# Performance work log

Measured on AMD Instinct MI355X. Metric: run time of the kernel, lower is better.

## Reference

```python
import jax, jax.numpy as jnp
import numpy as np

# Model dims
B = 64            # scenes (memory batch)
APER = 16         # agents per scene (uniform `length`)
A = B * APER      # total agents = sum(length)
TPAST = 20
TFUT = 30         # len_future
C = 256           # controller_size
M = 128           # memory_m
N = 256           # memory_n
H = 5             # num_heads (future modes)
SPACE = N // APER # per-agent write slot band
EMB = 16
D = C + M         # decoder hidden size


def _gru(x, h, wih, whh, bih, bhh):
    """torch.nn.GRU single-cell step."""
    gi = x @ wih.T + bih
    gh = h @ whh.T + bhh
    ir, iz, inn = jnp.split(gi, 3, axis=-1)
    hr, hz, hn = jnp.split(gh, 3, axis=-1)
    r = jax.nn.sigmoid(ir + hr)
    z = jax.nn.sigmoid(iz + hz)
    n = jnp.tanh(inn + r * hn)
    return (1.0 - z) * n + z * h


def _address(k, beta, mem, mask):
    """NTM content addressing: beta-sharpened masked softmax over cosine sims.
    k: (...,B,APER,M), beta: (...,B,APER,1), mem: (B,N,M), mask: (APER,N)."""
    kn = k / (jnp.linalg.norm(k, axis=-1, keepdims=True) + 1e-16)
    mn = mem / (jnp.linalg.norm(mem, axis=-1, keepdims=True) + 1e-16)
    sim = jnp.einsum('...bam,bnm->...ban', kn, mn)
    logits = beta * sim + (mask - 1.0) * 1e9
    return jax.nn.softmax(logits, axis=-1)


def setup_inputs() -> dict:
    key = jax.random.key(0)
    ks = iter(jax.random.split(key, 64))
    def nrm(shape, scale):
        return jax.random.normal(next(ks), shape, dtype=jnp.float32) * scale
    inp = dict(
        past=nrm((A, TPAST, 2), 1.0),
        past_rel=nrm((A, TPAST, 2), 1.0),
        ep_w1=nrm((8, 2), 0.7), ep_b1=jnp.zeros(8), ep_w2=nrm((EMB, 8), 0.35), ep_b2=jnp.zeros(EMB),
        er_w1=nrm((8, 2), 0.7), er_b1=jnp.zeros(8), er_w2=nrm((EMB, 8), 0.35), er_b2=jnp.zeros(EMB),
        enc_wih=nrm((3 * C, EMB + M), 1.0 / np.sqrt(EMB + M)), enc_whh=nrm((3 * C, C), 1.0 / np.sqrt(C)),
        enc_bih=jnp.zeros(3 * C), enc_bhh=jnp.zeros(3 * C),
        rel_wih=nrm((3 * C, EMB), 1.0 / np.sqrt(EMB)), rel_whh=nrm((3 * C, C), 1.0 / np.sqrt(C)),
        rel_bih=jnp.zeros(3 * C), rel_bhh=jnp.zeros(3 * C),
        dec_wih=nrm((3 * D, D), 1.0 / np.sqrt(D)), dec_whh=nrm((3 * D, D), 1.0 / np.sqrt(D)),
        dec_bih=jnp.zeros(3 * D), dec_bhh=jnp.zeros(3 * D),
        out_w=nrm((2, D), 1.0 / np.sqrt(D)), out_b=jnp.zeros(2),
        read_w=nrm((H, M + 1, C), 1.0 / np.sqrt(C)), read_b=jnp.zeros((H, M + 1)),
        write_w=nrm((3 * M + 1, C), 1.0 / np.sqrt(C)), write_b=jnp.zeros(3 * M + 1),
        init_r=nrm((1, M), 0.01),
        h_bias=nrm((1, C), 0.05), h_rel_bias=nrm((1, C), 0.05), h_fut_bias=nrm((1, D), 0.05),
        mem_bias=nrm((N, M), 0.05),
    )
    return inp


def reference(past, past_rel, ep_w1, ep_b1, ep_w2, ep_b2, er_w1, er_b1, er_w2, er_b2,
              enc_wih, enc_whh, enc_bih, enc_bhh, rel_wih, rel_whh, rel_bih, rel_bhh,
              dec_wih, dec_whh, dec_bih, dec_bhh, out_w, out_b,
              read_w, read_b, write_w, write_b,
              init_r, h_bias, h_rel_bias, h_fut_bias, mem_bias):
    # Per-agent disjoint write bands; read mask = other agents' bands.
    owner = jnp.arange(N) // SPACE
    mask_w = (owner[None, :] == jnp.arange(APER)[:, None]).astype(jnp.float32)  # (APER,N)
    mask_r = 1.0 - mask_w

    def mlp(x, w1, b1, w2, b2):
        return jax.nn.relu(x @ w1.T + b1) @ w2.T + b2

    emb_p = jnp.transpose(mlp(past, ep_w1, ep_b1, ep_w2, ep_b2), (1, 0, 2))      # (T,A,16)
    emb_r = jnp.transpose(mlp(past_rel, er_w1, er_b1, er_w2, er_b2), (1, 0, 2))  # (T,A,16)

    def step(carry, xs):
        emb, embr = xs
        mem, h, hr, hf, r = carry
        h = _gru(jnp.concatenate([emb, r], axis=-1), h, enc_wih, enc_whh, enc_bih, enc_bhh)
        hr = _gru(embr, hr, rel_wih, rel_whh, rel_bih, rel_bhh)
        # write head: k, beta, erase, add
        wp = h @ write_w.T + write_b
        kw = jnp.tanh(wp[:, :M]).reshape(B, APER, M)
        betaw = jax.nn.softplus(wp[:, M:M + 1]).reshape(B, APER, 1)
        er = jax.nn.sigmoid(wp[:, M + 1:2 * M + 1]).reshape(B, APER, M)
        ad = jnp.tanh(wp[:, 2 * M + 1:]).reshape(B, APER, M)
        ww = _address(kw, betaw, mem, mask_w)                                    # (B,APER,N)
        # erase/add; write bands are disjoint across agents so aggregation is exact
        mem = mem * (1.0 - jnp.einsum('ban,bam->bnm', ww, er)) + jnp.einsum('ban,bam->bnm', ww, ad)
        # per-head reads
        rp = jnp.einsum('ac,hkc->hak', hr, read_w) + read_b[:, None, :]          # (H,A,M+1)
        kr = jnp.tanh(rp[..., :M]).reshape(H, B, APER, M)
        betar = jax.nn.softplus(rp[..., M:]).reshape(H, B, APER, 1)
        wr = _address(kr, betar, mem, mask_r)                                    # (H,B,APER,N)
        reads = jnp.einsum('hban,bnm->hbam', wr, mem).reshape(H, A, M)
        r = reads[0]
        # per-mode decoder
        dec_in = jnp.concatenate([jnp.broadcast_to(h[None], (H, A, C)), reads], axis=-1).reshape(H * A, D)
        hf = _gru(dec_in, hf, dec_wih, dec_whh, dec_bih, dec_bhh)
        out = (hf @ out_w.T + out_b).reshape(H, A, 2)
        return (mem, h, hr, hf, r), out

    carry0 = (jnp.broadcast_to(mem_bias[None], (B, N, M)),
              jnp.broadcast_to(h_bias, (A, C)),
              jnp.broadcast_to(h_rel_bias, (A, C)),
              jnp.broadcast_to(h_fut_bias, (H * A, D)),
              jnp.broadcast_to(init_r, (A, M)))
    carry, _ = jax.lax.scan(step, carry0, (emb_p, emb_r))
    zf = jnp.zeros((TFUT, A, EMB), dtype=past.dtype)
    carry, outs = jax.lax.scan(step, carry, (zf, zf))                            # (TFUT,H,A,2)
    pred_rel = jnp.transpose(outs, (2, 1, 0, 3))                                 # (A,H,TFUT,2)
    pred = past[:, -1][:, None, None, :] + jnp.cumsum(pred_rel, axis=2)
    return pred, pred_rel
```

## Files before the change

### kernel.cpp

```cpp
#include <hip/hip_runtime.h>
#include <math.h>

#define B_    64
#define APER_ 16
#define A_    1024
#define TPAST_ 20
#define TFUT_  30
#define C_    256
#define M_    128
#define N_    256
#define H_    5
#define EMB_  16
#define D_    384
#define TTOT_ 50

typedef short bf16x8 __attribute__((ext_vector_type(8)));
typedef float f32x4 __attribute__((ext_vector_type(4)));

__device__ __forceinline__ float sigmoidf_(float x) { return 1.0f / (1.0f + expf(-x)); }
__device__ __forceinline__ float softplusf_(float x) { return (x > 20.0f) ? x : log1pf(expf(x)); }
__device__ __forceinline__ unsigned short f2bf(float f) {
    unsigned u = __float_as_uint(f);
    return (unsigned short)((u + 0x7FFFu + ((u >> 16) & 1u)) >> 16);
}
__device__ __forceinline__ float bf2f(short s) {
    return __uint_as_float(((unsigned)(unsigned short)s) << 16);
}

struct Cvt { const float* src; short* dst; int rows, sk, dk, total; };
struct Cvt8 { Cvt c[8]; };

__global__ __launch_bounds__(256) void convert_all(Cvt8 p)
{
    const int stride = gridDim.x * 256;
    #pragma unroll
    for (int s = 0; s < 8; ++s) {
        const Cvt d = p.c[s];
        for (int idx = blockIdx.x * 256 + threadIdx.x; idx < d.total; idx += stride) {
            const int r = idx / d.dk, k = idx % d.dk;
            float v = (k < d.sk && r < d.rows) ? d.src[(size_t)r * d.sk + k] : 0.f;
            d.dst[idx] = (short)f2bf(v);
        }
    }
}

__global__ __launch_bounds__(256) void embed2_k(const float* __restrict__ past, const float* __restrict__ past_rel,
                                                const float* __restrict__ pw1, const float* __restrict__ pb1,
                                                const float* __restrict__ pw2, const float* __restrict__ pb2,
                                                const float* __restrict__ rw1, const float* __restrict__ rb1,
                                                const float* __restrict__ rw2, const float* __restrict__ rb2,
                                                short* __restrict__ emb_p, short* __restrict__ emb_r)
{
    const int idx0 = blockIdx.x * 256 + threadIdx.x;
    const int half = A_ * TPAST_;
    if (idx0 >= 2 * half) return;
    const bool second = idx0 >= half;
    const int idx = second ? idx0 - half : idx0;
    const float* x = second ? past_rel : past;
    const float* w1 = second ? rw1 : pw1; const float* b1 = second ? rb1 : pb1;
    const float* w2 = second ? rw2 : pw2; const float* b2 = second ? rb2 : pb2;
    short* emb = second ? emb_r : emb_p;

    const int a = idx / TPAST_, t = idx % TPAST_;
    const float x0 = x[(size_t)idx * 2], x1 = x[(size_t)idx * 2 + 1];
    float hbuf[8];
    #pragma unroll
    for (int j = 0; j < 8; ++j) hbuf[j] = fmaxf(0.f, w1[j * 2] * x0 + w1[j * 2 + 1] * x1 + b1[j]);
    short* e = emb + ((size_t)t * A_ + a) * EMB_;
    #pragma unroll
    for (int i = 0; i < 16; ++i) {
        float acc = b2[i];
        #pragma unroll
        for (int j = 0; j < 8; ++j) acc += w2[i * 8 + j] * hbuf[j];
        e[i] = (short)f2bf(acc);
    }
}

__global__ __launch_bounds__(256) void init_k(float* __restrict__ h, const float* __restrict__ h_bias, short* __restrict__ hb,
                                              float* __restrict__ hr, const float* __restrict__ hr_bias, short* __restrict__ hrb,
                                              const float* __restrict__ hf_bias, short* __restrict__ hfb,
                                              short* __restrict__ reads_b, const float* __restrict__ init_r,
                                              short* __restrict__ memhi, short* __restrict__ memlo,
                                              float* __restrict__ normsG, const float* __restrict__ mem_bias)
{
    const int idx = blockIdx.x * 256 + threadIdx.x;
    if (idx < B_ * N_ * M_) {
        const float v = mem_bias[idx & (N_ * M_ - 1)];
        const short hv = (short)f2bf(v);
        memhi[idx] = hv;
        memlo[idx] = (short)f2bf(v - bf2f(hv));
    }
    if (idx < B_ * N_) {
        const float* r = mem_bias + (size_t)(idx & (N_ - 1)) * M_;
        float ss = 0.f;
        for (int k = 0; k < M_; ++k) ss += r[k] * r[k];
        normsG[idx] = sqrtf(ss) + 1e-16f;
    }
    if (idx < A_ * C_) {
        float v = h_bias[idx & (C_ - 1)];
        h[idx] = v; hb[idx] = (short)f2bf(v);
        v = hr_bias[idx & (C_ - 1)];
        hr[idx] = v; hrb[idx] = (short)f2bf(v);
    }
    if (idx < H_ * A_ * D_) {
        hfb[idx] = (short)f2bf(hf_bias[idx % D_]);
    }
    if (idx < A_ * M_) reads_b[idx] = (short)f2bf(init_r[idx & (M_ - 1)]);
}

__device__ __forceinline__ void gru_tile_split(
    int role, float* __restrict__ xchLane,
    const short* __restrict__ X1, int K1,
    const short* __restrict__ X2, int K2,
    const short* __restrict__ Wih, int Kpad,
    const float* __restrict__ bih,
    const short* __restrict__ Hb, const short* __restrict__ Whh,
    const float* __restrict__ bhh,
    const float* __restrict__ Hprev,
    float* __restrict__ Hnew, short* __restrict__ Hnewb,
    int G, int rowBase, int colBase, int lane)
{
    const int l16 = lane & 15;
    const int kb8 = (lane >> 4) * 8;
    const f32x4 z4 = {0.f, 0.f, 0.f, 0.f};
    f32x4 a0[2][2], a1[2][2], a2[2][2];
    #pragma unroll
    for (int i = 0; i < 2; ++i)
        #pragma unroll
        for (int j = 0; j < 2; ++j) { a0[i][j] = z4; a1[i][j] = z4; a2[i][j] = z4; }

    if (role == 0) {
        for (int kc = 0; kc < Kpad; kc += 32) {
            const int k8 = kc + kb8;
            bf16x8 ax[2];
            #pragma unroll
            for (int i = 0; i < 2; ++i) {
                const int r = rowBase + i * 16 + l16;
                bf16x8 v = {0, 0, 0, 0, 0, 0, 0, 0};
                if (k8 < K1) {
                    if (X1) v = *(const bf16x8*)(X1 + (size_t)(r & 1023) * K1 + k8);
                } else if (k8 < K1 + K2) {
                    v = *(const bf16x8*)(X2 + (size_t)r * K2 + (k8 - K1));
                }
                ax[i] = v;
            }
            #pragma unroll
            for (int j = 0; j < 2; ++j) {
                const size_t wb = (size_t)(colBase + j * 16 + l16) * Kpad + k8;
                const bf16x8 b0 = *(const bf16x8*)(Wih + wb);
                const bf16x8 b1 = *(const bf16x8*)(Wih + (size_t)G * Kpad + wb);
                const bf16x8 b2 = *(const bf16x8*)(Wih + (size_t)2 * G * Kpad + wb);
                a0[0][j] = __builtin_amdgcn_mfma_f32_16x16x32_bf16(ax[0], b0, a0[0][j], 0, 0, 0);
                a0[1][j] = __builtin_amdgcn_mfma_f32_16x16x32_bf16(ax[1], b0, a0[1][j], 0, 0, 0);
                a1[0][j] = __builtin_amdgcn_mfma_f32_16x16x32_bf16(ax[0], b1, a1[0][j], 0, 0, 0);
                a1[1][j] = __builtin_amdgcn_mfma_f32_16x16x32_bf16(ax[1], b1, a1[1][j], 0, 0, 0);
                a2[0][j] = __builtin_amdgcn_mfma_f32_16x16x32_bf16(ax[0], b2, a2[0][j], 0, 0, 0);
                a2[1][j] = __builtin_amdgcn_mfma_f32_16x16x32_bf16(ax[1], b2, a2[1][j], 0, 0, 0);
            }
        }
        #pragma unroll
        for (int i = 0; i < 2; ++i)
            #pragma unroll
            for (int j = 0; j < 2; ++j)
                #pragma unroll
                for (int q = 0; q < 4; ++q) {
                    const int base = (i * 2 + j) * 4 + q;
                    xchLane[base]      = a0[i][j][q];
                    xchLane[16 + base] = a1[i][j][q];
                    xchLane[32 + base] = a2[i][j][q];
                }
    } else {
        for (int kc = 0; kc < G; kc += 32) {
            const int k8 = kc + kb8;
            bf16x8 ah[2];
            #pragma unroll
            for (int i = 0; i < 2; ++i)
                ah[i] = *(const bf16x8*)(Hb + (size_t)(rowBase + i * 16 + l16) * G + k8);
            #pragma unroll
            for (int j = 0; j < 2; ++j) {
                const size_t wb = (size_t)(colBase + j * 16 + l16) * G + k8;
                const bf16x8 b0 = *(const bf16x8*)(Whh + wb);
                const bf16x8 b1 = *(const bf16x8*)(Whh + (size_t)G * G + wb);
                const bf16x8 b2 = *(const bf16x8*)(Whh + (size_t)2 * G * G + wb);
                a0[0][j] = __builtin_amdgcn_mfma_f32_16x16x32_bf16(ah[0], b0, a0[0][j], 0, 0, 0);
                a0[1][j] = __builtin_amdgcn_mfma_f32_16x16x32_bf16(ah[1], b0, a0[1][j], 0, 0, 0);
                a1[0][j] = __builtin_amdgcn_mfma_f32_16x16x32_bf16(ah[0], b1, a1[0][j], 0, 0, 0);
                a1[1][j] = __builtin_amdgcn_mfma_f32_16x16x32_bf16(ah[1], b1, a1[1][j], 0, 0, 0);
                a2[0][j] = __builtin_amdgcn_mfma_f32_16x16x32_bf16(ah[0], b2, a2[0][j], 0, 0, 0);
                a2[1][j] = __builtin_amdgcn_mfma_f32_16x16x32_bf16(ah[1], b2, a2[1][j], 0, 0, 0);
            }
        }
    }
    __syncthreads();
    if (role != 1) return;

    const int r4 = (lane >> 4) * 4;
    #pragma unroll
    for (int j = 0; j < 2; ++j) {
        const int col = colBase + j * 16 + l16;
        const float b0c = bih[col] + bhh[col];
        const float b1c = bih[G + col] + bhh[G + col];
        const float bi2 = bih[2 * G + col], bh2 = bhh[2 * G + col];
        #pragma unroll
        for (int i = 0; i < 2; ++i) {
            #pragma unroll
            for (int q = 0; q < 4; ++q) {
                const int row = rowBase + i * 16 + r4 + q;
                const int base = (i * 2 + j) * 4 + q;
                const float arv = a0[i][j][q] + xchLane[base];
                const float azv = a1[i][j][q] + xchLane[16 + base];
                const float aniv = xchLane[32 + base];
                const float anhv = a2[i][j][q];
                const float rr = sigmoidf_(arv + b0c);
                const float zz = sigmoidf_(azv + b1c);
                const float nn = tanhf(aniv + bi2 + rr * (anhv + bh2));
                const float hp = Hprev ? Hprev[(size_t)row * G + col]
                                       : bf2f(Hb[(size_t)row * G + col]);
                const float hv = (1.f - zz) * nn + zz * hp;
                if (Hnew) Hnew[(size_t)row * G + col] = hv;
                Hnewb[(size_t)row * G + col] = (short)f2bf(hv);
            }
        }
    }
}

__device__ __forceinline__ void gemm_tile(
    const short* __restrict__ Xb, const short* __restrict__ Wb,
    const float* __restrict__ bias, float* __restrict__ Out,
    int Ncols, int K, int rowBase, int colBase, int lane)
{
    const int l16 = lane & 15;
    const int kb8 = (lane >> 4) * 8;
    const f32x4 z4 = {0.f, 0.f, 0.f, 0.f};
    f32x4 acc[2][2] = {{z4, z4}, {z4, z4}};

    for (int kc = 0; kc < K; kc += 32) {
        const int k8 = kc + kb8;
        const bf16x8 a0 = *(const bf16x8*)(Xb + (size_t)(rowBase + l16) * K + k8);
        const bf16x8 a1 = *(const bf16x8*)(Xb + (size_t)(rowBase + 16 + l16) * K + k8);
        const bf16x8 b0 = *(const bf16x8*)(Wb + (size_t)(colBase + l16) * K + k8);
        const bf16x8 b1 = *(const bf16x8*)(Wb + (size_t)(colBase + 16 + l16) * K + k8);
        acc[0][0] = __builtin_amdgcn_mfma_f32_16x16x32_bf16(a0, b0, acc[0][0], 0, 0, 0);
        acc[0][1] = __builtin_amdgcn_mfma_f32_16x16x32_bf16(a0, b1, acc[0][1], 0, 0, 0);
        acc[1][0] = __builtin_amdgcn_mfma_f32_16x16x32_bf16(a1, b0, acc[1][0], 0, 0, 0);
        acc[1][1] = __builtin_amdgcn_mfma_f32_16x16x32_bf16(a1, b1, acc[1][1], 0, 0, 0);
    }
    const int r4 = (lane >> 4) * 4;
    #pragma unroll
    for (int j = 0; j < 2; ++j) {
        const int col = colBase + j * 16 + l16;
        if (col >= Ncols) continue;
        const float bv = bias[col];
        #pragma unroll
        for (int i = 0; i < 2; ++i)
            #pragma unroll
            for (int q = 0; q < 4; ++q) {
                const int row = rowBase + i * 16 + r4 + q;
                Out[(size_t)row * Ncols + col] = acc[i][j][q] + bv;
            }
    }
}

__global__ __launch_bounds__(256) void phaseA(
    const short* __restrict__ ep, const short* __restrict__ er,
    const short* __restrict__ enc_wih, const float* __restrict__ enc_bih,
    const short* __restrict__ enc_whh, const float* __restrict__ enc_bhh,
    const short* __restrict__ rel_wih, const float* __restrict__ rel_bih,
    const short* __restrict__ rel_whh, const float* __restrict__ rel_bhh,
    const short* __restrict__ dec_wih, const float* __restrict__ dec_bih,
    const short* __restrict__ dec_whh, const float* __restrict__ dec_bhh,
    const float* __restrict__ hc, const short* __restrict__ hbc,
    float* __restrict__ hn, short* __restrict__ hbn,
    const float* __restrict__ hrc, const short* __restrict__ hrbc,
    float* __restrict__ hrn, short* __restrict__ hrbn,
    const short* __restrict__ hfbc, short* __restrict__ hfbn,
    const short* __restrict__ reads_b,
    int decBlocks, int encBlocks)
{
    __shared__ float xch[2][64][49];
    const int bid = blockIdx.x;
    const int wv = threadIdx.x >> 6;
    const int lane = threadIdx.x & 63;
    const int pair = wv >> 1, role = wv & 1;
    float* xchLane = &xch[pair][lane][0];

    if (bid < decBlocks) {
        const int tile = bid * 2 + pair;
        gru_tile_split(role, xchLane,
                       hbc, 256, reads_b, 128, dec_wih, 384, dec_bih,
                       hfbc, dec_whh, dec_bhh, nullptr, nullptr, hfbn, D_,
                       (tile / 12) * 32, (tile % 12) * 32, lane);
    } else if (bid < decBlocks + encBlocks) {
        const int tile = (bid - decBlocks) * 2 + pair;
        gru_tile_split(role, xchLane,
                       ep, 16, reads_b, 128, enc_wih, 160, enc_bih,
                       hbc, enc_whh, enc_bhh, hc, hn, hbn, C_,
                       (tile >> 3) * 32, (tile & 7) * 32, lane);
    } else {
        const int tile = (bid - decBlocks - encBlocks) * 2 + pair;
        gru_tile_split(role, xchLane,
                       er, 16, nullptr, 0, rel_wih, 32, rel_bih,
                       hrbc, rel_whh, rel_bhh, hrc, hrn, hrbn, C_,
                       (tile >> 3) * 32, (tile & 7) * 32, lane);
    }
}

__global__ __launch_bounds__(256) void phaseHeads(
    const short* __restrict__ hbn, const short* __restrict__ write_w_b,
    const float* __restrict__ write_b, float* __restrict__ wp,
    const short* __restrict__ hrbn, const short* __restrict__ read_w_b,
    const float* __restrict__ read_b, float* __restrict__ rp,
    const short* __restrict__ hfbn, const float* __restrict__ out_w,
    const float* __restrict__ out_b, float* __restrict__ predrel,
    int outT, int wpBlocks, int rpBlocks)
{
    const int bid = blockIdx.x;
    const int wave = threadIdx.x >> 6;
    const int lane = threadIdx.x & 63;

    if (bid < wpBlocks) {
        const int tile = bid * 4 + wave;
        gemm_tile(hbn, write_w_b, write_b, wp, 385, C_,
                  (tile & 31) * 32, (tile >> 5) * 32, lane);
    } else if (bid < wpBlocks + rpBlocks) {
        const int tile = (bid - wpBlocks) * 4 + wave;
        gemm_tile(hrbn, read_w_b, read_b, rp, 645, C_,
                  (tile & 31) * 32, (tile >> 5) * 32, lane);
    } else {
        const int widx = (bid - wpBlocks - rpBlocks) * 4 + wave;
        const int g = lane >> 3, li = lane & 7;
        const int row = widx * 8 + g;
        const short* hrow = hfbn + (size_t)row * D_;
        float a0 = 0.f, a1 = 0.f;
        #pragma unroll
        for (int u = 0; u < 6; ++u) {
            const int k0 = u * 64 + li * 8;
            const bf16x8 v = *(const bf16x8*)(hrow + k0);
            #pragma unroll
            for (int r = 0; r < 8; ++r) {
                const float f = bf2f(v[r]);
                a0 = fmaf(f, out_w[k0 + r], a0);
                a1 = fmaf(f, out_w[D_ + k0 + r], a1);
            }
        }
        a0 += __shfl_xor(a0, 1); a0 += __shfl_xor(a0, 2); a0 += __shfl_xor(a0, 4);
        a1 += __shfl_xor(a1, 1); a1 += __shfl_xor(a1, 2); a1 += __shfl_xor(a1, 4);
        if (li == 0) {
            const int hh = row >> 10, aa = row & 1023;
            float* o = predrel + (((size_t)aa * H_ + hh) * TFUT_ + outT) * 2;
            o[0] = a0 + out_b[0];
            o[1] = a1 + out_b[1];
        }
    }
}

__global__ __launch_bounds__(256) void write_mem_k(const float* __restrict__ wp,
                                                   short* __restrict__ memhi, short* __restrict__ memlo,
                                                   float* __restrict__ normsG)
{
    const int a = blockIdx.x;
    const int b = a >> 4, p = a & 15;
    __shared__ float kw[128], er[128], ad[128], red[256], ww[16], logit[16];
    __shared__ float buf[2048];
    __shared__ float beta_s, knorm_s;
    const int tid = threadIdx.x;
    const float* w = wp + (size_t)a * 385;
    if (tid < 128) {
        kw[tid] = tanhf(w[tid]);
        er[tid] = sigmoidf_(w[129 + tid]);
        ad[tid] = tanhf(w[257 + tid]);
    }
    if (tid == 0) beta_s = softplusf_(w[128]);
    __syncthreads();

    red[tid] = (tid < 128) ? kw[tid] * kw[tid] : 0.f;
    __syncthreads();
    for (int s = 128; s > 0; s >>= 1) { if (tid < s) red[tid] += red[tid + s]; __syncthreads(); }
    if (tid == 0) knorm_s = sqrtf(red[0]) + 1e-16f;
    __syncthreads();

    const int s = tid >> 4, j = tid & 15;
    float dot = 0.f, ss = 0.f;
    {
        const size_t row = (size_t)(b * N_) + p * 16 + s;
        const short* hi = memhi + row * M_;
        const short* lo = memlo + row * M_;
        for (int k = j; k < 128; k += 16) {
            const float v = bf2f(hi[k]) + bf2f(lo[k]);
            dot += kw[k] * v; ss += v * v;
        }
    }
    red[tid] = dot; __syncthreads();
    for (int st = 8; st > 0; st >>= 1) { if (j < st) red[tid] += red[tid + st]; __syncthreads(); }
    float dotf = red[s * 16];
    __syncthreads();
    red[tid] = ss; __syncthreads();
    for (int st = 8; st > 0; st >>= 1) { if (j < st) red[tid] += red[tid + st]; __syncthreads(); }
    float ssf = red[s * 16];
    if (j == 0) {
        float mn = sqrtf(ssf) + 1e-16f;
        logit[s] = beta_s * (dotf / (mn * knorm_s));
    }
    __syncthreads();
    if (tid == 0) {
        float mx = -1e30f;
        for (int i = 0; i < 16; ++i) mx = fmaxf(mx, logit[i]);
        float sum = 0.f;
        for (int i = 0; i < 16; ++i) { float e = __expf(logit[i] - mx); ww[i] = e; sum += e; }
        float inv = 1.f / sum;
        for (int i = 0; i < 16; ++i) ww[i] *= inv;
    }
    __syncthreads();
    for (int idx = tid; idx < 16 * 128; idx += 256) {
        int si = idx >> 7, m = idx & 127;
        size_t g = ((size_t)(b * N_) + p * 16 + si) * M_ + m;
        float wwv = ww[si];
        const float old = bf2f(memhi[g]) + bf2f(memlo[g]);
        float v = old * (1.f - wwv * er[m]) + wwv * ad[m];
        const short hv = (short)f2bf(v);
        memhi[g] = hv;
        memlo[g] = (short)f2bf(v - bf2f(hv));
        buf[idx] = v;
    }
    __syncthreads();
    {
        float ssq = 0.f;
        #pragma unroll
        for (int i = 0; i < 8; ++i) { float v = buf[s * 128 + j + 16 * i]; ssq += v * v; }
        #pragma unroll
        for (int m = 1; m < 16; m <<= 1) ssq += __shfl_xor(ssq, m);
        if (j == 0) normsG[b * N_ + p * 16 + s] = sqrtf(ssq) + 1e-16f;
    }
}

__global__ __launch_bounds__(256) void read_k2(const float* __restrict__ rp,
                                               const short* __restrict__ memhi,
                                               const short* __restrict__ memlo,
                                               const float* __restrict__ normsG,
                                               short* __restrict__ reads_b)
{
    const int b = blockIdx.x;
    const int h = blockIdx.y;
    __shared__ __align__(16) float kq[16 * 132];
    __shared__ float S[16 * 260];
    __shared__ float beta_s[16], knorm_s[16], inv_s[16];
    const int t = threadIdx.x;
    const int a = t >> 4;
    const int sub = t & 15;

    {
        const float* base = rp + ((size_t)(b * 16 + a)) * 645 + h * 129;
        const int k0 = sub * 8;
        float v[8]; float ss = 0.f;
        #pragma unroll
        for (int r = 0; r < 8; ++r) { v[r] = tanhf(base[k0 + r]); ss += v[r] * v[r]; }
        float* dst = kq + a * 132 + k0;
        *(float4*)dst = make_float4(v[0], v[1], v[2], v[3]);
        *(float4*)(dst + 4) = make_float4(v[4], v[5], v[6], v[7]);
        #pragma unroll
        for (int m = 1; m < 16; m <<= 1) ss += __shfl_xor(ss, m);
        if (sub == 0) {
            knorm_s[a] = sqrtf(ss) + 1e-16f;
            beta_s[a] = softplusf_(base[128]);
        }
    }
    __syncthreads();

    {
        const int wave = t >> 6, lane = t & 63;
        const int l16 = lane & 15, kb8 = (lane >> 4) * 8;
        const int slotBase = wave * 64;
        const f32x4 z4 = {0.f, 0.f, 0.f, 0.f};
        f32x4 acc[4] = {z4, z4, z4, z4};
        const short* mbh = memhi + (size_t)b * N_ * M_;
        const short* mbl = memlo + (size_t)b * N_ * M_;
        #pragma unroll
        for (int kc = 0; kc < 128; kc += 32) {
            const float* ap = kq + l16 * 132 + kc + kb8;
            bf16x8 ah, al;
            #pragma unroll
            for (int r = 0; r < 8; ++r) {
                const float av = ap[r];
                const short hv = (short)f2bf(av);
                ah[r] = hv; al[r] = (short)f2bf(av - bf2f(hv));
            }
            #pragma unroll
            for (int tt = 0; tt < 4; ++tt) {
                const size_t roff = (size_t)(slotBase + tt * 16 + l16) * M_ + kc + kb8;
                const bf16x8 bh = *(const bf16x8*)(mbh + roff);
                const bf16x8 bl = *(const bf16x8*)(mbl + roff);
                acc[tt] = __builtin_amdgcn_mfma_f32_16x16x32_bf16(ah, bh, acc[tt], 0, 0, 0);
                acc[tt] = __builtin_amdgcn_mfma_f32_16x16x32_bf16(ah, bl, acc[tt], 0, 0, 0);
                acc[tt] = __builtin_amdgcn_mfma_f32_16x16x32_bf16(al, bh, acc[tt], 0, 0, 0);
            }
        }
        const int r4 = (lane >> 4) * 4;
        #pragma unroll
        for (int tt = 0; tt < 4; ++tt) {
            const int slot = slotBase + tt * 16 + l16;
            const float nv = normsG[b * N_ + slot];
            #pragma unroll
            for (int q = 0; q < 4; ++q) {
                const int aq = r4 + q;
                const float lg = ((slot >> 4) == aq) ? -1e30f
                               : beta_s[aq] * acc[tt][q] / (nv * knorm_s[aq]);
                S[aq * 260 + slot] = lg;
            }
        }
    }
    __syncthreads();

    {
        float mx = -1e30f;
        #pragma unroll
        for (int i = 0; i < 16; ++i) mx = fmaxf(mx, S[a * 260 + sub + 16 * i]);
        #pragma unroll
        for (int m = 1; m < 16; m <<= 1) mx = fmaxf(mx, __shfl_xor(mx, m));
        float e[16]; float sum = 0.f;
        #pragma unroll
        for (int i = 0; i < 16; ++i) { e[i] = __expf(S[a * 260 + sub + 16 * i] - mx); sum += e[i]; }
        #pragma unroll
        for (int i = 0; i < 16; ++i) S[a * 260 + sub + 16 * i] = e[i];
        #pragma unroll
        for (int m = 1; m < 16; m <<= 1) sum += __shfl_xor(sum, m);
        if (sub == 0) inv_s[a] = 1.f / sum;
    }
    __syncthreads();

    {
        const int m0 = sub * 8;
        const short* mbh = memhi + (size_t)b * N_ * M_ + m0;
        const short* mbl = memlo + (size_t)b * N_ * M_ + m0;
        float acc[8];
        #pragma unroll
        for (int r = 0; r < 8; ++r) acc[r] = 0.f;
        const float* Sa = S + a * 260;
        #pragma unroll 2
        for (int n = 0; n < N_; ++n) {
            const float w = Sa[n];
            const bf16x8 vh = *(const bf16x8*)(mbh + (size_t)n * M_);
            const bf16x8 vl = *(const bf16x8*)(mbl + (size_t)n * M_);
            #pragma unroll
            for (int r = 0; r < 8; ++r)
                acc[r] = fmaf(w, bf2f(vh[r]) + bf2f(vl[r]), acc[r]);
        }
        const float inv = inv_s[a];
        short pk[8];
        #pragma unroll
        for (int r = 0; r < 8; ++r) pk[r] = (short)f2bf(acc[r] * inv);
        *(bf16x8*)(reads_b + ((size_t)h * A_ + b * 16 + a) * M_ + m0) = *(bf16x8*)pk;
    }
}

__global__ __launch_bounds__(256) void cumsum_k(const float* __restrict__ past,
                                                const float* __restrict__ predrel,
                                                float* __restrict__ pred)
{
    const int idx = blockIdx.x * 256 + threadIdx.x;
    if (idx >= A_ * H_ * 2) return;
    const int c = idx & 1;
    const int ah = idx >> 1;
    const int a = ah / H_;
    float acc = past[((size_t)a * TPAST_ + TPAST_ - 1) * 2 + c];
    const float* pr = predrel + (size_t)ah * TFUT_ * 2 + c;
    float* pd = pred + (size_t)ah * TFUT_ * 2 + c;
    for (int t = 0; t < TFUT_; ++t) { acc += pr[t * 2]; pd[t * 2] = acc; }
}

extern "C" void kernel_launch(void* const* d_in, const int* in_sizes, int n_in,
                              void* d_out, int out_size, void* d_ws, size_t ws_size,
                              hipStream_t stream)
{
    const float* past       = (const float*)d_in[0];
    const float* past_rel   = (const float*)d_in[1];
    const float* ep_w1      = (const float*)d_in[2];
    const float* ep_b1      = (const float*)d_in[3];
    const float* ep_w2      = (const float*)d_in[4];
    const float* ep_b2      = (const float*)d_in[5];
    const float* er_w1      = (const float*)d_in[6];
    const float* er_b1      = (const float*)d_in[7];
    const float* er_w2      = (const float*)d_in[8];
    const float* er_b2      = (const float*)d_in[9];
    const float* enc_wih    = (const float*)d_in[10];
    const float* enc_whh    = (const float*)d_in[11];
    const float* enc_bih    = (const float*)d_in[12];
    const float* enc_bhh    = (const float*)d_in[13];
    const float* rel_wih    = (const float*)d_in[14];
    const float* rel_whh    = (const float*)d_in[15];
    const float* rel_bih    = (const float*)d_in[16];
    const float* rel_bhh    = (const float*)d_in[17];
    const float* dec_wih    = (const float*)d_in[18];
    const float* dec_whh    = (const float*)d_in[19];
    const float* dec_bih    = (const float*)d_in[20];
    const float* dec_bhh    = (const float*)d_in[21];
    const float* out_w      = (const float*)d_in[22];
    const float* out_b      = (const float*)d_in[23];
    const float* read_w     = (const float*)d_in[24];
    const float* read_b     = (const float*)d_in[25];
    const float* write_w    = (const float*)d_in[26];
    const float* write_b    = (const float*)d_in[27];
    const float* init_r     = (const float*)d_in[28];
    const float* h_bias     = (const float*)d_in[29];
    const float* h_rel_bias = (const float*)d_in[30];
    const float* h_fut_bias = (const float*)d_in[31];
    const float* mem_bias   = (const float*)d_in[32];

    float* pred    = (float*)d_out;
    float* predrel = pred + (size_t)A_ * H_ * TFUT_ * 2;

    float* ws = (float*)d_ws;
    size_t off = 0;
    auto alloc = [&](size_t n) { float* p = ws + off; off += n; return p; };
    float* h0     = alloc((size_t)A_ * C_);
    float* h1     = alloc((size_t)A_ * C_);
    float* hr0    = alloc((size_t)A_ * C_);
    float* hr1    = alloc((size_t)A_ * C_);
    float* wp     = alloc((size_t)A_ * 385);
    float* rp     = alloc((size_t)A_ * 645);
    float* normsG = alloc((size_t)B_ * N_);

    short* sws = (short*)(ws + off);
    size_t soff = 0;
    auto salloc = [&](size_t n) { short* p = sws + soff; soff += n; return p; };
    short* emb_p_b   = salloc((size_t)TPAST_ * A_ * EMB_);
    short* emb_r_b   = salloc((size_t)TPAST_ * A_ * EMB_);
    short* hb0       = salloc((size_t)A_ * C_);
    short* hb1       = salloc((size_t)A_ * C_);
    short* hrb0      = salloc((size_t)A_ * C_);
    short* hrb1      = salloc((size_t)A_ * C_);
    short* hfb0      = salloc((size_t)H_ * A_ * D_);
    short* hfb1      = salloc((size_t)H_ * A_ * D_);
    short* reads_b   = salloc((size_t)H_ * A_ * M_);
    short* memhi     = salloc((size_t)B_ * N_ * M_);
    short* memlo     = salloc((size_t)B_ * N_ * M_);
    short* enc_wih_b = salloc((size_t)768 * 160);
    short* enc_whh_b = salloc((size_t)768 * 256);
    short* rel_wih_b = salloc((size_t)768 * 32);
    short* rel_whh_b = salloc((size_t)768 * 256);
    short* dec_wih_b = salloc((size_t)1152 * 384);
    short* dec_whh_b = salloc((size_t)1152 * 384);
    short* write_w_b = salloc((size_t)416 * 256);
    short* read_w_b  = salloc((size_t)672 * 256);
    (void)ws_size; (void)in_sizes; (void)n_in; (void)out_size;

    Cvt8 cp;
    cp.c[0] = {enc_wih, enc_wih_b, 768, 144, 160, 768 * 160};
    cp.c[1] = {enc_whh, enc_whh_b, 768, 256, 256, 768 * 256};
    cp.c[2] = {rel_wih, rel_wih_b, 768, 16, 32, 768 * 32};
    cp.c[3] = {rel_whh, rel_whh_b, 768, 256, 256, 768 * 256};
    cp.c[4] = {dec_wih, dec_wih_b, 1152, 384, 384, 1152 * 384};
    cp.c[5] = {dec_whh, dec_whh_b, 1152, 384, 384, 1152 * 384};
    cp.c[6] = {write_w, write_w_b, 385, 256, 256, 416 * 256};
    cp.c[7] = {read_w, read_w_b, 645, 256, 256, 672 * 256};
    convert_all<<<1024, 256, 0, stream>>>(cp);

    init_k<<<(B_ * N_ * M_ + 255) / 256, 256, 0, stream>>>(
        h0, h_bias, hb0, hr0, h_rel_bias, hrb0, h_fut_bias, hfb0,
        reads_b, init_r, memhi, memlo, normsG, mem_bias);
    embed2_k<<<(2 * A_ * TPAST_ + 255) / 256, 256, 0, stream>>>(
        past, past_rel, ep_w1, ep_b1, ep_w2, ep_b2, er_w1, er_b1, er_w2, er_b2,
        emb_p_b, emb_r_b);

    float *hc = h0, *hn = h1, *hrc = hr0, *hrn = hr1;
    short *hbc = hb0, *hbn = hb1, *hrbc = hrb0, *hrbn = hrb1, *hfbc = hfb0, *hfbn = hfb1;

    const dim3 g_read(B_, H_);

    for (int t = 0; t < TTOT_; ++t) {
        const short* ep = (t < TPAST_) ? emb_p_b + (size_t)t * A_ * EMB_ : nullptr;
        const short* er = (t < TPAST_) ? emb_r_b + (size_t)t * A_ * EMB_ : nullptr;

        const int decBlocks = (t == 0) ? 0 : 960;
        phaseA<<<decBlocks + 256, 256, 0, stream>>>(
            ep, er,
            enc_wih_b, enc_bih, enc_whh_b, enc_bhh,
            rel_wih_b, rel_bih, rel_whh_b, rel_bhh,
            dec_wih_b, dec_bih, dec_whh_b, dec_bhh,
            hc, hbc, hn, hbn,
            hrc, hrbc, hrn, hrbn,
            hfbc, hfbn,
            reads_b, decBlocks, 128);

        const int gridH = (t >= 21) ? 432 : 272;
        phaseHeads<<<gridH, 256, 0, stream>>>(
            hbn, write_w_b, write_b, wp,
            hrbn, read_w_b, read_b, rp,
            hfbn, out_w, out_b, predrel, t - 21, 104, 168);

        write_mem_k<<<A_, 256, 0, stream>>>(wp, memhi, memlo, normsG);

        read_k2<<<g_read, 256, 0, stream>>>(rp, memhi, memlo, normsG, reads_b);

        float* tf; short* ts;
        tf = hc; hc = hn; hn = tf;       ts = hbc; hbc = hbn; hbn = ts;
        tf = hrc; hrc = hrn; hrn = tf;   ts = hrbc; hrbc = hrbn; hrbn = ts;
        if (t >= 1) {
            ts = hfbc; hfbc = hfbn; hfbn = ts;
        }
    }

    phaseA<<<960, 256, 0, stream>>>(
        nullptr, nullptr,
        enc_wih_b, enc_bih, enc_whh_b, enc_bhh,
        rel_wih_b, rel_bih, rel_whh_b, rel_bhh,
        dec_wih_b, dec_bih, dec_whh_b, dec_bhh,
        hc, hbc, hn, hbn,
        hrc, hrbc, hrn, hrbn,
        hfbc, hfbn,
        reads_b, 960, 0);
    phaseHeads<<<160, 256, 0, stream>>>(
        hbn, write_w_b, write_b, wp,
        hrbn, read_w_b, read_b, rp,
        hfbn, out_w, out_b, predrel, TFUT_ - 1, 0, 0);
    cumsum_k<<<(A_ * H_ * 2 + 255) / 256, 256, 0, stream>>>(past, predrel, pred);
}
```

Baseline: 6.022 ms.

## Remap GRU tiles for XCD-local weight reuse and use nontemporal hidden-state access

Remaps decoder, encoder and relational GRU tile indices so that consecutive block IDs, which round-robin across the 8 XCDs, give each XCD a contiguous column band. Each XCD's L2 then holds only a slice of the weight matrices. Decoder hidden-state reads and writes, and the output head's reads, become nontemporal loads and stores so these streaming activations do not evict cached weights. The added index arithmetic is small. The nontemporal hints may hurt if the hidden state would have been reused from cache.

```diff
diff --git a/kernel.cpp b/kernel.cpp
--- a/kernel.cpp
+++ b/kernel.cpp
@@ -108,6 +108,7 @@
     if (idx < A_ * M_) reads_b[idx] = (short)f2bf(init_r[idx & (M_ - 1)]);
 }
 
+template <bool NTH>
 __device__ __forceinline__ void gru_tile_split(
     int role, float* __restrict__ xchLane,
     const short* __restrict__ X1, int K1,
@@ -174,8 +175,10 @@
             const int k8 = kc + kb8;
             bf16x8 ah[2];
             #pragma unroll
-            for (int i = 0; i < 2; ++i)
-                ah[i] = *(const bf16x8*)(Hb + (size_t)(rowBase + i * 16 + l16) * G + k8);
+            for (int i = 0; i < 2; ++i) {
+                const bf16x8* p = (const bf16x8*)(Hb + (size_t)(rowBase + i * 16 + l16) * G + k8);
+                ah[i] = NTH ? __builtin_nontemporal_load(p) : *p;
+            }
             #pragma unroll
             for (int j = 0; j < 2; ++j) {
                 const size_t wb = (size_t)(colBase + j * 16 + l16) * G + k8;
@@ -214,11 +217,15 @@
                 const float rr = sigmoidf_(arv + b0c);
                 const float zz = sigmoidf_(azv + b1c);
                 const float nn = tanhf(aniv + bi2 + rr * (anhv + bh2));
-                const float hp = Hprev ? Hprev[(size_t)row * G + col]
-                                       : bf2f(Hb[(size_t)row * G + col]);
+                float hp;
+                if (Hprev) hp = Hprev[(size_t)row * G + col];
+                else if (NTH) hp = bf2f(__builtin_nontemporal_load(Hb + (size_t)row * G + col));
+                else hp = bf2f(Hb[(size_t)row * G + col]);
                 const float hv = (1.f - zz) * nn + zz * hp;
                 if (Hnew) Hnew[(size_t)row * G + col] = hv;
-                Hnewb[(size_t)row * G + col] = (short)f2bf(hv);
+                const short hs = (short)f2bf(hv);
+                if (NTH) __builtin_nontemporal_store(hs, Hnewb + (size_t)row * G + col);
+                else Hnewb[(size_t)row * G + col] = hs;
             }
         }
     }
@@ -285,23 +292,29 @@
     float* xchLane = &xch[pair][lane][0];
 
     if (bid < decBlocks) {
-        const int tile = bid * 2 + pair;
-        gru_tile_split(role, xchLane,
+        const int x = bid & 7, j = bid >> 3;
+        const int ct = x * 240 + j * 2 + pair;
+        const int rowT = ct % 160, colT = ct / 160;
+        gru_tile_split<true>(role, xchLane,
                        hbc, 256, reads_b, 128, dec_wih, 384, dec_bih,
                        hfbc, dec_whh, dec_bhh, nullptr, nullptr, hfbn, D_,
-                       (tile / 12) * 32, (tile % 12) * 32, lane);
+                       rowT * 32, colT * 32, lane);
     } else if (bid < decBlocks + encBlocks) {
-        const int tile = (bid - decBlocks) * 2 + pair;
-        gru_tile_split(role, xchLane,
+        const int e = bid - decBlocks;
+        const int x = e & 7, j = e >> 3;
+        const int ct = x * 32 + j * 2 + pair;
+        gru_tile_split<false>(role, xchLane,
                        ep, 16, reads_b, 128, enc_wih, 160, enc_bih,
                        hbc, enc_whh, enc_bhh, hc, hn, hbn, C_,
-                       (tile >> 3) * 32, (tile & 7) * 32, lane);
+                       (ct % 32) * 32, (ct / 32) * 32, lane);
     } else {
-        const int tile = (bid - decBlocks - encBlocks) * 2 + pair;
-        gru_tile_split(role, xchLane,
+        const int e = bid - decBlocks - encBlocks;
+        const int x = e & 7, j = e >> 3;
+        const int ct = x * 32 + j * 2 + pair;
+        gru_tile_split<false>(role, xchLane,
                        er, 16, nullptr, 0, rel_wih, 32, rel_bih,
                        hrbc, rel_whh, rel_bhh, hrc, hrn, hrbn, C_,
-                       (tile >> 3) * 32, (tile & 7) * 32, lane);
+                       (ct % 32) * 32, (ct / 32) * 32, lane);
     }
 }
 
@@ -335,7 +348,7 @@
         #pragma unroll
         for (int u = 0; u < 6; ++u) {
             const int k0 = u * 64 + li * 8;
-            const bf16x8 v = *(const bf16x8*)(hrow + k0);
+            const bf16x8 v = __builtin_nontemporal_load((const bf16x8*)(hrow + k0));
             #pragma unroll
             for (int r = 0; r < 8; ++r) {
                 const float f = bf2f(v[r]);
```

New measurement: 6.757 ms. 1.12x slower.
